# Performance work log

Hardware: AMD Instinct MI355X
Metric: run time of the kernel (lower is better)

Reference implementation:

```python
import jax, jax.numpy as jnp
import numpy as np

EMB = 1024
HID = 4 * EMB
HEADS = 16
HEAD_DIM = EMB // HEADS


def gelu_tanh(x):
    c = jnp.sqrt(jnp.asarray(2.0 / jnp.pi, x.dtype))
    return 0.5 * x * (1.0 + jnp.tanh(c * (x + 0.044715 * x ** 3)))


def layernorm(x, scale, shift, eps=1e-5):
    mean = jnp.mean(x, axis=-1, keepdims=True)
    var = jnp.var(x, axis=-1, keepdims=True)
    return scale * (x - mean) / jnp.sqrt(var + eps) + shift


def setup_inputs() -> dict:
    key = jax.random.key(0)
    ks = jax.random.split(key, 12)
    s = 0.02
    return {
        "x": jax.random.normal(ks[0], (2, 2048, EMB), jnp.float32),
        "Wq": jax.random.normal(ks[1], (EMB, EMB), jnp.float32) * s,
        "Wk": jax.random.normal(ks[2], (EMB, EMB), jnp.float32) * s,
        "Wv": jax.random.normal(ks[3], (EMB, EMB), jnp.float32) * s,
        "Wo": jax.random.normal(ks[4], (EMB, EMB), jnp.float32) * s,
        "bo": jnp.zeros((EMB,), jnp.float32),
        "W1": jax.random.normal(ks[5], (EMB, HID), jnp.float32) * s,
        "b1": jnp.zeros((HID,), jnp.float32),
        "W2": jax.random.normal(ks[6], (HID, EMB), jnp.float32) * s,
        "b2": jnp.zeros((EMB,), jnp.float32),
        "ln1_scale": jnp.ones((EMB,), jnp.float32),
        "ln1_shift": jnp.zeros((EMB,), jnp.float32),
        "ln2_scale": jnp.ones((EMB,), jnp.float32),
        "ln2_shift": jnp.zeros((EMB,), jnp.float32),
    }


def reference(x, Wq, Wk, Wv, Wo, bo, W1, b1, W2, b2,
              ln1_scale, ln1_shift, ln2_scale, ln2_shift):
    B, S, D = x.shape

    # pre-norm attention + residual
    h = layernorm(x, ln1_scale, ln1_shift)
    q = (h @ Wq).reshape(B, S, HEADS, HEAD_DIM).transpose(0, 2, 1, 3)  # bhsd
    k = (h @ Wk).reshape(B, S, HEADS, HEAD_DIM).transpose(0, 2, 1, 3)
    v = (h @ Wv).reshape(B, S, HEADS, HEAD_DIM).transpose(0, 2, 1, 3)

    scores = jnp.einsum("bhqd,bhkd->bhqk", q, k)
    causal = jnp.tril(jnp.ones((S, S), bool))
    scores = jnp.where(causal, scores, -jnp.inf)
    attn = jax.nn.softmax(scores / jnp.sqrt(jnp.asarray(HEAD_DIM, x.dtype)), axis=-1)
    ctx = jnp.einsum("bhqk,bhkd->bhqd", attn, v)
    ctx = ctx.transpose(0, 2, 1, 3).reshape(B, S, D)
    x = x + (ctx @ Wo + bo)

    # pre-norm FFN + residual
    h = layernorm(x, ln2_scale, ln2_shift)
    h = gelu_tanh(h @ W1 + b1) @ W2 + b2
    return x + h
```

## Files before the change

kernel.cpp:

```cpp
#include <hip/hip_runtime.h>
#include <hip/hip_bf16.h>
#include <stdint.h>

#define B_   2
#define S_   2048
#define D_   1024
#define H_   16
#define DH_  64
#define HID_ 4096
#define M_   4096

typedef __bf16 bf16x8 __attribute__((ext_vector_type(8)));
typedef float  f32x4  __attribute__((ext_vector_type(4)));
typedef float  f32x16 __attribute__((ext_vector_type(16)));
typedef uint32_t u32x4v __attribute__((ext_vector_type(4)));

typedef const uint32_t __attribute__((address_space(1))) u32g;
typedef uint32_t       __attribute__((address_space(3))) u32l;

#define SCL2K_ 0.18033688011112042f

__device__ __forceinline__ uint16_t f2bf(float f) {
  uint32_t u = __builtin_bit_cast(uint32_t, f);
  u += 0x7FFFu + ((u >> 16) & 1u);
  return (uint16_t)(u >> 16);
}

__device__ __forceinline__ float bf2f(uint16_t u) {
  return __builtin_bit_cast(float, (uint32_t)u << 16);
}

__device__ __forceinline__ void gload_lds16(const void* g, void* l) {
  __builtin_amdgcn_global_load_lds((u32g*)g, (u32l*)l, 16, 0, 0);
}

__device__ __forceinline__ const bf16x8* lds8p(const uint16_t* base, int row,
                                               int cole) {
  int byt = (cole * 2) ^ ((row & 7) << 4);
  return reinterpret_cast<const bf16x8*>(base + row * 64 + (byt >> 1));
}

__device__ __forceinline__ uint32_t cvtpk_bf16(float lo, float hi) {
  uint32_t d;
  asm("v_cvt_pk_bf16_f32 %0, %1, %2" : "=v"(d) : "v"(lo), "v"(hi));
  return d;
}
__device__ __forceinline__ void pl32swap(uint32_t& a, uint32_t& b) {
  asm volatile("v_permlane32_swap_b32 %0, %1" : "+v"(a), "+v"(b));
}

__global__ void wconv_t(const float* __restrict__ W, uint16_t* __restrict__ WT,
                        int K, int N) {
  __shared__ float tile[32][33];
  int n0 = blockIdx.x * 32, k0 = blockIdx.y * 32;
  int tx = threadIdx.x, ty = threadIdx.y;
#pragma unroll
  for (int i = 0; i < 4; ++i)
    tile[ty + i * 8][tx] = W[(size_t)(k0 + ty + i * 8) * N + n0 + tx];
  __syncthreads();
#pragma unroll
  for (int i = 0; i < 4; ++i)
    WT[(size_t)(n0 + ty + i * 8) * K + k0 + tx] = f2bf(tile[tx][ty + i * 8]);
}

__global__ __launch_bounds__(256) void ln_k(const float* __restrict__ x,
                                            const float* __restrict__ sc,
                                            const float* __restrict__ sh,
                                            uint16_t* __restrict__ out) {
  int row = blockIdx.x;
  int t = threadIdx.x;
  float4 v = reinterpret_cast<const float4*>(x + (size_t)row * D_)[t];
  float s = v.x + v.y + v.z + v.w;
  float ss = v.x * v.x + v.y * v.y + v.z * v.z + v.w * v.w;
#pragma unroll
  for (int off = 32; off >= 1; off >>= 1) {
    s += __shfl_xor(s, off);
    ss += __shfl_xor(ss, off);
  }
  __shared__ float red[8];
  int wid = t >> 6, lane = t & 63;
  if (lane == 0) { red[wid] = s; red[wid + 4] = ss; }
  __syncthreads();
  s = red[0] + red[1] + red[2] + red[3];
  ss = red[4] + red[5] + red[6] + red[7];
  float mean = s * (1.0f / D_);
  float var = ss * (1.0f / D_) - mean * mean;
  float rstd = rsqrtf(var + 1e-5f);
  float4 g = reinterpret_cast<const float4*>(sc)[t];
  float4 b = reinterpret_cast<const float4*>(sh)[t];
  ushort4 o;
  o.x = f2bf(g.x * (v.x - mean) * rstd + b.x);
  o.y = f2bf(g.y * (v.y - mean) * rstd + b.y);
  o.z = f2bf(g.z * (v.z - mean) * rstd + b.z);
  o.w = f2bf(g.w * (v.w - mean) * rstd + b.w);
  reinterpret_cast<ushort4*>(out + (size_t)row * D_)[t] = o;
}

__global__ __launch_bounds__(256) void reduce4_k(
    const uint16_t* __restrict__ P0, const uint16_t* __restrict__ P1,
    const uint16_t* __restrict__ P2, const uint16_t* __restrict__ P3,
    const float* __restrict__ resid, const float* __restrict__ bias,
    float* __restrict__ out) {
  int row = blockIdx.x, t = threadIdx.x;
  size_t base = (size_t)row * D_ + t * 4;
  float4 r = *reinterpret_cast<const float4*>(resid + base);
  float4 b = reinterpret_cast<const float4*>(bias)[t];
  ushort4 u0 = *reinterpret_cast<const ushort4*>(P0 + base);
  ushort4 u1 = *reinterpret_cast<const ushort4*>(P1 + base);
  ushort4 u2 = *reinterpret_cast<const ushort4*>(P2 + base);
  ushort4 u3 = *reinterpret_cast<const ushort4*>(P3 + base);
  float4 o;
  o.x = r.x + b.x + bf2f(u0.x) + bf2f(u1.x) + bf2f(u2.x) + bf2f(u3.x);
  o.y = r.y + b.y + bf2f(u0.y) + bf2f(u1.y) + bf2f(u2.y) + bf2f(u3.y);
  o.z = r.z + b.z + bf2f(u0.z) + bf2f(u1.z) + bf2f(u2.z) + bf2f(u3.z);
  o.w = r.w + b.w + bf2f(u0.w) + bf2f(u1.w) + bf2f(u2.w) + bf2f(u3.w);
  *reinterpret_cast<float4*>(out + base) = o;
}

__global__ void vtrans_k(const uint16_t* __restrict__ V, uint16_t* __restrict__ VT) {
  __shared__ uint16_t tile[32][33];
  int s0 = blockIdx.x * 32, d0 = blockIdx.y * 32, bh = blockIdx.z;
  int tx = threadIdx.x, ty = threadIdx.y;
  const uint16_t* vb = V + (size_t)bh * S_ * DH_;
  uint16_t* vtb = VT + (size_t)bh * DH_ * S_;
#pragma unroll
  for (int i = 0; i < 4; ++i)
    tile[ty + i * 8][tx] = vb[(size_t)(s0 + ty + i * 8) * DH_ + d0 + tx];
  __syncthreads();
#pragma unroll
  for (int i = 0; i < 4; ++i)
    vtb[(size_t)(d0 + ty + i * 8) * S_ + s0 + tx] = tile[tx][ty + i * 8];
}

template <int EPI>
__global__ __launch_bounds__(512, 2) void gemm8(
    const uint16_t* __restrict__ A, const uint16_t* __restrict__ BT,
    void* __restrict__ Cout, const float* __restrict__ bias,
    uint16_t* __restrict__ P0, uint16_t* __restrict__ P1,
    uint16_t* __restrict__ P2, uint16_t* __restrict__ P3,
    int M, int N, int K) {
  __shared__ uint16_t As[2][2][128 * 64];
  __shared__ uint16_t Bs[2][2][128 * 64];
  int t = threadIdx.x;
  int lane = t & 63, wid = t >> 6;
  int wm = wid >> 2, wn = wid & 3;
  int l15 = lane & 15, lk8 = (lane >> 4) * 8, lr4 = (lane >> 4) * 4;
  int gx = gridDim.x;
  int nwg = gx * gridDim.y;
  int bid = blockIdx.y * gx + blockIdx.x;
  int swz = (bid & 7) * (nwg >> 3) + (bid >> 3);
  int bx = swz % gx, by = swz / gx;
  int m0 = by * 256, n0 = bx * 256;
  int ksz = K / gridDim.z;
  int kbeg = blockIdx.z * ksz;
  int NT = ksz >> 6;

  int r0 = t >> 3, slot0 = t & 7;
  int scol = (slot0 ^ (r0 & 7)) * 8;

  auto STAGE_A = [&](int kt, int half, int buf) {
    const uint16_t* src =
        A + (size_t)(m0 + half * 128 + r0) * K + kbeg + kt * 64 + scol;
    uint16_t* dst = &As[buf][half][t * 8];
    gload_lds16(src, dst);
    gload_lds16(src + (size_t)64 * K, dst + 4096);
  };
  auto STAGE_B = [&](int kt, int half, int buf) {
    const uint16_t* src =
        BT + (size_t)(n0 + half * 128 + r0) * K + kbeg + kt * 64 + scol;
    uint16_t* dst = &Bs[buf][half][t * 8];
    gload_lds16(src, dst);
    gload_lds16(src + (size_t)64 * K, dst + 4096);
  };

  bf16x8 a[4][2], b[2][2];
  auto LDA = [&](int buf, int mh) {
#pragma unroll
    for (int j = 0; j < 4; ++j)
#pragma unroll
      for (int kk = 0; kk < 2; ++kk)
        a[j][kk] = *lds8p(As[buf][mh], wm * 64 + j * 16 + l15, kk * 32 + lk8);
  };
  auto LDB = [&](int buf, int nh) {
#pragma unroll
    for (int jj = 0; jj < 2; ++jj)
#pragma unroll
      for (int kk = 0; kk < 2; ++kk)
        b[jj][kk] = *lds8p(Bs[buf][nh], wn * 32 + jj * 16 + l15, kk * 32 + lk8);
  };

  f32x4 acc[8][4] = {};
  auto MM = [&](int mh, int nh) {
    __builtin_amdgcn_s_setprio(1);
#pragma unroll
    for (int kk = 0; kk < 2; ++kk)
#pragma unroll
      for (int j = 0; j < 4; ++j)
#pragma unroll
        for (int jj = 0; jj < 2; ++jj)
          acc[mh * 4 + j][nh * 2 + jj] = __builtin_amdgcn_mfma_f32_16x16x32_bf16(
              a[j][kk], b[jj][kk], acc[mh * 4 + j][nh * 2 + jj], 0, 0, 0);
    __builtin_amdgcn_s_setprio(0);
  };
  auto BAR = [&]() {
    __builtin_amdgcn_s_barrier();
    asm volatile("" ::: "memory");
  };
  auto LGKM0 = [&]() {
    asm volatile("s_waitcnt lgkmcnt(0)" ::: "memory");
    __builtin_amdgcn_sched_barrier(0);
  };

  STAGE_A(0, 0, 0);
  STAGE_B(0, 1, 0);
  STAGE_B(0, 0, 0);
  STAGE_A(0, 1, 0);
  STAGE_A(1, 0, 1);
  STAGE_B(1, 1, 1);
  asm volatile("s_waitcnt vmcnt(4)" ::: "memory");
  BAR();

  for (int T = 0; T < NT; ++T) {
    int cur = T & 1;
    LDA(cur, 0);
    LDB(cur, 0);
    if (T + 1 < NT) STAGE_B(T + 1, 0, cur ^ 1);
    BAR(); LGKM0();
    MM(0, 0);
    BAR();
    LDB(cur, 1);
    if (T + 1 < NT) STAGE_A(T + 1, 1, cur ^ 1);
    BAR(); LGKM0();
    MM(0, 1);
    BAR();
    LDA(cur, 1);
    if (T + 2 < NT) STAGE_A(T + 2, 0, cur);
    BAR(); LGKM0();
    MM(1, 1);
    BAR();
    LDB(cur, 0);
    if (T + 2 < NT) STAGE_B(T + 2, 1, cur);
    BAR(); LGKM0();
    MM(1, 0);
    if (T + 1 < NT) {
      if (T == NT - 2) {
        asm volatile("s_waitcnt vmcnt(0)" ::: "memory");
      } else {
        asm volatile("s_waitcnt vmcnt(4)" ::: "memory");
      }
    }
    BAR();
  }

  uint16_t* Pz = nullptr;
  if constexpr (EPI == 3) {
    int z = blockIdx.z;
    Pz = (z == 0) ? P0 : (z == 1) ? P1 : (z == 2) ? P2 : P3;
  }
#pragma unroll
  for (int mi = 0; mi < 8; ++mi) {
#pragma unroll
    for (int ni = 0; ni < 4; ++ni) {
#pragma unroll
      for (int rr = 0; rr < 4; ++rr) {
        int gm = m0 + (mi >> 2) * 128 + wm * 64 + (mi & 3) * 16 + lr4 + rr;
        int gn = n0 + (ni >> 1) * 128 + wn * 32 + (ni & 1) * 16 + l15;
        float v = acc[mi][ni][rr];
        if constexpr (EPI == 0) {
          int which = gn >> 10, nc = gn & 1023;
          int h = nc >> 6, dh = nc & 63;
          int bb = gm >> 11, s = gm & 2047;
          if (which == 1) v *= SCL2K_;
          ((uint16_t*)Cout)[((size_t)which * 32 + bb * 16 + h) * (S_ * 64) +
                            (size_t)s * 64 + dh] = f2bf(v);
        } else if constexpr (EPI == 2) {
          float u = v + bias[gn];
          float y = 0.7978845608028654f * (u + 0.044715f * u * u * u);
          float e = __expf(2.0f * y);
          float th = 1.0f - 2.0f / (e + 1.0f);
          ((uint16_t*)Cout)[(size_t)gm * N + gn] = f2bf(0.5f * u * (1.0f + th));
        } else {
          Pz[(size_t)gm * N + gn] = f2bf(v);
        }
      }
    }
  }
}

template <int EPI>
__global__ __launch_bounds__(256) void gemm_bt(
    const uint16_t* __restrict__ A, const uint16_t* __restrict__ BT,
    void* __restrict__ Cout, const float* __restrict__ bias,
    const float* __restrict__ resid, int M, int N, int K) {
  __shared__ uint16_t Asm_[128 * 64];
  __shared__ uint16_t Bsm_[128 * 64];
  int t = threadIdx.x;
  int lane = t & 63, wid = t >> 6;
  int wr = wid >> 1, wc = wid & 1;
  int nwg = gridDim.x * gridDim.y;
  int bid = blockIdx.y * gridDim.x + blockIdx.x;
  int swz = (bid & 7) * (nwg >> 3) + (bid >> 3);
  int bx = swz % gridDim.x, by = swz / gridDim.x;
  int m0 = by * 128, n0 = bx * 128;
  int l15 = lane & 15, lk8 = (lane >> 4) * 8;
  f32x4 acc[4][4] = {};

  auto STAGE = [&](int k0) {
#pragma unroll
    for (int it = 0; it < 4; ++it) {
      int idx = it * 256 + t;
      int r = idx >> 3, slot = idx & 7;
      int c = (slot ^ (r & 7)) * 8;
      gload_lds16(A + (size_t)(m0 + r) * K + k0 + c, &Asm_[idx * 8]);
      gload_lds16(BT + (size_t)(n0 + r) * K + k0 + c, &Bsm_[idx * 8]);
    }
  };

  int niter = K >> 6;
  for (int ki = 0; ki < niter; ++ki) {
    __syncthreads();
    STAGE(ki * 64);
    __syncthreads();
#pragma unroll
    for (int kk = 0; kk < 2; ++kk) {
      bf16x8 a[4], b[4];
#pragma unroll
      for (int mi = 0; mi < 4; ++mi)
        a[mi] = *lds8p(Asm_, wr * 64 + mi * 16 + l15, kk * 32 + lk8);
#pragma unroll
      for (int ni = 0; ni < 4; ++ni)
        b[ni] = *lds8p(Bsm_, wc * 64 + ni * 16 + l15, kk * 32 + lk8);
#pragma unroll
      for (int mi = 0; mi < 4; ++mi)
#pragma unroll
        for (int ni = 0; ni < 4; ++ni)
          acc[mi][ni] = __builtin_amdgcn_mfma_f32_16x16x32_bf16(
              a[mi], b[ni], acc[mi][ni], 0, 0, 0);
    }
  }
  int lr4 = (lane >> 4) * 4;
#pragma unroll
  for (int mi = 0; mi < 4; ++mi) {
#pragma unroll
    for (int ni = 0; ni < 4; ++ni) {
#pragma unroll
      for (int r = 0; r < 4; ++r) {
        int gm = m0 + wr * 64 + mi * 16 + lr4 + r;
        int gn = n0 + wc * 64 + ni * 16 + l15;
        float v = acc[mi][ni][r];
        if constexpr (EPI == 1) {
          ((float*)Cout)[(size_t)gm * N + gn] =
              resid[(size_t)gm * N + gn] + v + bias[gn];
        }
      }
    }
  }
}

__global__ __launch_bounds__(64) void attn32_k(const uint16_t* __restrict__ Q,
                                               const uint16_t* __restrict__ Kv,
                                               const uint16_t* __restrict__ VT,
                                               uint16_t* __restrict__ ctx) {
  __shared__ uint16_t Ksm[2][32 * 64];
  __shared__ uint16_t Vsm[2][32 * 64];
  __shared__ float invLDS[2][32];
  int bid = blockIdx.x;
  int wgrp = bid >> 3;
  int j = wgrp & 31;
  int bh = (bid & 7) + 8 * (wgrp >> 5);
  int lane = threadIdx.x;
  int l31 = lane & 31, lh = lane >> 5;
  int b_ = bh >> 4, h_ = bh & 15;

  auto STAGE = [&](int k0, int bufi) {
#pragma unroll
    for (int c = 0; c < 4; ++c) {
      int idx = c * 64 + lane;
      int r = idx >> 3, sl = idx & 7;
      int slp = sl ^ (r & 7);
      gload_lds16(Kv + ((size_t)bh * S_ + k0 + r) * 64 + slp * 8,
                  &Ksm[bufi][idx * 8]);
      int dh = 2 * r + (slp >> 2), ko = (slp & 3) * 8;
      gload_lds16(VT + ((size_t)bh * 64 + dh) * S_ + k0 + ko,
                  &Vsm[bufi][idx * 8]);
    }
  };

  int buf = 0;
  STAGE(0, 0);

  for (int half = 0; half < 2; ++half) {
    int qt = half ? (63 - j) : j;
    int nkt = qt + 1;
    int qbase = qt * 32;
    bf16x8 qf[4];
#pragma unroll
    for (int dk = 0; dk < 4; ++dk)
      qf[dk] = *reinterpret_cast<const bf16x8*>(
          Q + ((size_t)bh * S_ + qbase + l31) * 64 + dk * 16 + lh * 8);
    f32x16 o0 = {}, o1 = {};
    float mrow = -3.0e38f, lsum = 0.0f;

    for (int t = 0; t < nkt; ++t) {
      if (t + 1 < nkt) {
        STAGE((t + 1) * 32, buf ^ 1);
        asm volatile("s_waitcnt vmcnt(8)" ::: "memory");
      } else if (half == 0) {
        STAGE(0, buf ^ 1);
        asm volatile("s_waitcnt vmcnt(8)" ::: "memory");
      } else {
        asm volatile("s_waitcnt vmcnt(0)" ::: "memory");
      }
      __builtin_amdgcn_sched_barrier(0);
      f32x16 Sf = {};
#pragma unroll
      for (int dk = 0; dk < 4; ++dk) {
        bf16x8 kf = *lds8p(Ksm[buf], l31, dk * 16 + lh * 8);
        Sf = __builtin_amdgcn_mfma_f32_32x32x16_bf16(kf, qf[dk], Sf, 0, 0, 0);
      }
      float sv[16];
      if (t == nkt - 1) {
#pragma unroll
        for (int rr = 0; rr < 16; ++rr) {
          int koff = (rr & 3) + 8 * (rr >> 2) + 4 * lh;
          sv[rr] = (koff <= l31) ? Sf[rr] : -3.0e38f;
        }
      } else {
#pragma unroll
        for (int rr = 0; rr < 16; ++rr) sv[rr] = Sf[rr];
      }
      float mt = sv[0];
#pragma unroll
      for (int rr = 1; rr < 16; ++rr) mt = fmaxf(mt, sv[rr]);
#pragma unroll
      for (int off = 32; off >= 1; off >>= 1)
        mt = fmaxf(mt, __shfl_xor(mt, off));
      if (mt > mrow + 8.0f) {
        float fac = __builtin_amdgcn_exp2f(mrow - mt);
        mrow = mt;
        lsum *= fac;
#pragma unroll
        for (int rr = 0; rr < 16; ++rr) { o0[rr] *= fac; o1[rr] *= fac; }
      }
      float pv[16];
#pragma unroll
      for (int rr = 0; rr < 16; ++rr) {
        pv[rr] = __builtin_amdgcn_exp2f(sv[rr] - mrow);
        lsum += pv[rr];
      }
      uint32_t a0 = cvtpk_bf16(pv[0], pv[1]), b0 = cvtpk_bf16(pv[4], pv[5]);
      pl32swap(a0, b0);
      uint32_t a1 = cvtpk_bf16(pv[2], pv[3]), b1 = cvtpk_bf16(pv[6], pv[7]);
      pl32swap(a1, b1);
      u32x4v w0 = {a0, a1, b0, b1};
      bf16x8 pa0 = __builtin_bit_cast(bf16x8, w0);
      uint32_t a2 = cvtpk_bf16(pv[8], pv[9]), b2 = cvtpk_bf16(pv[12], pv[13]);
      pl32swap(a2, b2);
      uint32_t a3 = cvtpk_bf16(pv[10], pv[11]), b3 = cvtpk_bf16(pv[14], pv[15]);
      pl32swap(a3, b3);
      u32x4v w1 = {a2, a3, b2, b3};
      bf16x8 pa1 = __builtin_bit_cast(bf16x8, w1);
      int vrow = l31 >> 1, vcb = (l31 & 1) * 32 + lh * 8;
      bf16x8 v00 = *lds8p(Vsm[buf], vrow, vcb);
      o0 = __builtin_amdgcn_mfma_f32_32x32x16_bf16(pa0, v00, o0, 0, 0, 0);
      bf16x8 v01 = *lds8p(Vsm[buf], vrow, vcb + 16);
      o0 = __builtin_amdgcn_mfma_f32_32x32x16_bf16(pa1, v01, o0, 0, 0, 0);
      bf16x8 v10 = *lds8p(Vsm[buf], 16 + vrow, vcb);
      o1 = __builtin_amdgcn_mfma_f32_32x32x16_bf16(pa0, v10, o1, 0, 0, 0);
      bf16x8 v11 = *lds8p(Vsm[buf], 16 + vrow, vcb + 16);
      o1 = __builtin_amdgcn_mfma_f32_32x32x16_bf16(pa1, v11, o1, 0, 0, 0);
      buf ^= 1;
    }
    lsum += __shfl_xor(lsum, 32);
    if (lane < 32) invLDS[half][l31] = 1.0f / lsum;
    asm volatile("s_waitcnt lgkmcnt(0)" ::: "memory");
    __builtin_amdgcn_sched_barrier(0);
    float inv[16];
#pragma unroll
    for (int rr = 0; rr < 16; ++rr)
      inv[rr] = invLDS[half][(rr & 3) + 8 * (rr >> 2) + 4 * lh];
#pragma unroll
    for (int rr = 0; rr < 16; ++rr) {
      int s = qbase + (rr & 3) + 8 * (rr >> 2) + 4 * lh;
      size_t base = ((size_t)(b_ * S_ + s)) * D_ + h_ * 64;
      ctx[base + l31] = f2bf(o0[rr] * inv[rr]);
      ctx[base + 32 + l31] = f2bf(o1[rr] * inv[rr]);
    }
  }
}

extern "C" void kernel_launch(void* const* d_in, const int* in_sizes, int n_in,
                              void* d_out, int out_size, void* d_ws, size_t ws_size,
                              hipStream_t stream) {
  const float* x    = (const float*)d_in[0];
  const float* Wq   = (const float*)d_in[1];
  const float* Wk   = (const float*)d_in[2];
  const float* Wv   = (const float*)d_in[3];
  const float* Wo   = (const float*)d_in[4];
  const float* bo   = (const float*)d_in[5];
  const float* W1   = (const float*)d_in[6];
  const float* b1   = (const float*)d_in[7];
  const float* W2   = (const float*)d_in[8];
  const float* b2   = (const float*)d_in[9];
  const float* ln1s = (const float*)d_in[10];
  const float* ln1b = (const float*)d_in[11];
  const float* ln2s = (const float*)d_in[12];
  const float* ln2b = (const float*)d_in[13];
  float* out = (float*)d_out;
  char* ws = (char*)d_ws;

  const size_t MB = 1024 * 1024;
  uint16_t* WQKVT = (uint16_t*)(ws + 0);
  uint16_t* WOT   = (uint16_t*)(ws + 6 * MB);
  uint16_t* W1T   = (uint16_t*)(ws + 8 * MB);
  uint16_t* W2T   = (uint16_t*)(ws + 16 * MB);
  uint16_t* H1    = (uint16_t*)(ws + 24 * MB);
  float*    X1    = (float*)(ws + 32 * MB);
  uint16_t* QKV   = (uint16_t*)(ws + 48 * MB);
  uint16_t* VTb   = (uint16_t*)(ws + 72 * MB);
  uint16_t* CTX   = (uint16_t*)(ws + 80 * MB);
  uint16_t* FFH   = (uint16_t*)(ws + 48 * MB);
  uint16_t* SP0   = (uint16_t*)(ws + 0);
  uint16_t* SP1   = (uint16_t*)(ws + 8 * MB);
  uint16_t* SP2   = (uint16_t*)(ws + 24 * MB);
  uint16_t* SP3   = (uint16_t*)(ws + 80 * MB);

  dim3 b32x8(32, 8);
  wconv_t<<<dim3(32, 32), b32x8, 0, stream>>>(Wq, WQKVT, 1024, 1024);
  wconv_t<<<dim3(32, 32), b32x8, 0, stream>>>(Wk, WQKVT + 1024 * 1024, 1024, 1024);
  wconv_t<<<dim3(32, 32), b32x8, 0, stream>>>(Wv, WQKVT + 2 * 1024 * 1024, 1024, 1024);
  wconv_t<<<dim3(32, 32), b32x8, 0, stream>>>(Wo, WOT, 1024, 1024);
  wconv_t<<<dim3(128, 32), b32x8, 0, stream>>>(W1, W1T, 1024, 4096);
  wconv_t<<<dim3(32, 128), b32x8, 0, stream>>>(W2, W2T, 4096, 1024);

  ln_k<<<M_, 256, 0, stream>>>(x, ln1s, ln1b, H1);
  gemm8<0><<<dim3(12, 16), 512, 0, stream>>>(H1, WQKVT, QKV, nullptr,
                                             nullptr, nullptr, nullptr, nullptr,
                                             M_, 3072, 1024);
  const uint16_t* Qp = QKV;
  const uint16_t* Kp = QKV + (size_t)32 * S_ * 64;
  const uint16_t* Vp = QKV + (size_t)64 * S_ * 64;
  vtrans_k<<<dim3(64, 2, 32), b32x8, 0, stream>>>(Vp, VTb);
  attn32_k<<<dim3(1024), 64, 0, stream>>>(Qp, Kp, VTb, CTX);
  gemm_bt<1><<<dim3(8, 32), 256, 0, stream>>>(CTX, WOT, X1, bo, x, M_, 1024, 1024);
  ln_k<<<M_, 256, 0, stream>>>(X1, ln2s, ln2b, H1);
  gemm8<2><<<dim3(16, 16), 512, 0, stream>>>(H1, W1T, FFH, b1,
                                             nullptr, nullptr, nullptr, nullptr,
                                             M_, 4096, 1024);
  gemm8<3><<<dim3(4, 16, 4), 512, 0, stream>>>(FFH, W2T, nullptr, nullptr,
                                               SP0, SP1, SP2, SP3,
                                               M_, 1024, 4096);
  reduce4_k<<<M_, 256, 0, stream>>>(SP0, SP1, SP2, SP3, X1, b2, out);
}
```

Measured before the change: 269.7 us.

## Split paired causal attention blocks into one q-tile per block, tweak swizzle and rescale

The attention kernel stops giving each block two complementary query tiles (j and 63-j) for load balance. It now launches one block per query tile, doubling the grid to 2048 single-wave blocks, with heavy tiles scheduled last by block index. The LDS swizzle gains an extra XOR bit on row bit 3 to cut bank conflicts, and the online-softmax rescale check now uses a wave-wide __any before the cross-lane max reduction. This trades the explicit pairing for more parallelism and leaves it to the hardware scheduler to balance the uneven causal work.

New measurement: 256.5 us. 4.9% less time.

```diff
diff --git a/kernel.cpp b/kernel.cpp
--- a/kernel.cpp
+++ b/kernel.cpp
@@ -37,6 +37,12 @@
 __device__ __forceinline__ const bf16x8* lds8p(const uint16_t* base, int row,
                                                int cole) {
   int byt = (cole * 2) ^ ((row & 7) << 4);
+  return reinterpret_cast<const bf16x8*>(base + row * 64 + (byt >> 1));
+}
+
+__device__ __forceinline__ const bf16x8* lds8p32(const uint16_t* base, int row,
+                                                 int cole) {
+  int byt = (cole * 2) ^ ((row & 7) << 4) ^ ((row & 8) << 2);
   return reinterpret_cast<const bf16x8*>(base + row * 64 + (byt >> 1));
 }
 
@@ -363,11 +369,10 @@
                                                uint16_t* __restrict__ ctx) {
   __shared__ uint16_t Ksm[2][32 * 64];
   __shared__ uint16_t Vsm[2][32 * 64];
-  __shared__ float invLDS[2][32];
+  __shared__ float invLDS[32];
   int bid = blockIdx.x;
-  int wgrp = bid >> 3;
-  int j = wgrp & 31;
-  int bh = (bid & 7) + 8 * (wgrp >> 5);
+  int qt = bid >> 5;
+  int bh = bid & 31;
   int lane = threadIdx.x;
   int l31 = lane & 31, lh = lane >> 5;
   int b_ = bh >> 4, h_ = bh & 15;
@@ -377,7 +382,7 @@
     for (int c = 0; c < 4; ++c) {
       int idx = c * 64 + lane;
       int r = idx >> 3, sl = idx & 7;
-      int slp = sl ^ (r & 7);
+      int slp = sl ^ (r & 7) ^ ((r & 8) >> 2);
       gload_lds16(Kv + ((size_t)bh * S_ + k0 + r) * 64 + slp * 8,
                   &Ksm[bufi][idx * 8]);
       int dh = 2 * r + (slp >> 2), ko = (slp & 3) * 8;
@@ -386,106 +391,101 @@
     }
   };
 
+  int nkt = qt + 1;
+  int qbase = qt * 32;
+  bf16x8 qf[4];
+#pragma unroll
+  for (int dk = 0; dk < 4; ++dk)
+    qf[dk] = *reinterpret_cast<const bf16x8*>(
+        Q + ((size_t)bh * S_ + qbase + l31) * 64 + dk * 16 + lh * 8);
+  f32x16 o0 = {}, o1 = {};
+  float mrow = -3.0e38f, lsum = 0.0f;
   int buf = 0;
   STAGE(0, 0);
 
-  for (int half = 0; half < 2; ++half) {
-    int qt = half ? (63 - j) : j;
-    int nkt = qt + 1;
-    int qbase = qt * 32;
-    bf16x8 qf[4];
-#pragma unroll
-    for (int dk = 0; dk < 4; ++dk)
-      qf[dk] = *reinterpret_cast<const bf16x8*>(
-          Q + ((size_t)bh * S_ + qbase + l31) * 64 + dk * 16 + lh * 8);
-    f32x16 o0 = {}, o1 = {};
-    float mrow = -3.0e38f, lsum = 0.0f;
-
-    for (int t = 0; t < nkt; ++t) {
-      if (t + 1 < nkt) {
-        STAGE((t + 1) * 32, buf ^ 1);
-        asm volatile("s_waitcnt vmcnt(8)" ::: "memory");
-      } else if (half == 0) {
-        STAGE(0, buf ^ 1);
-        asm volatile("s_waitcnt vmcnt(8)" ::: "memory");
-      } else {
-        asm volatile("s_waitcnt vmcnt(0)" ::: "memory");
+  for (int t = 0; t < nkt; ++t) {
+    if (t + 1 < nkt) {
+      STAGE((t + 1) * 32, buf ^ 1);
+      asm volatile("s_waitcnt vmcnt(8)" ::: "memory");
+    } else {
+      asm volatile("s_waitcnt vmcnt(0)" ::: "memory");
+    }
+    __builtin_amdgcn_sched_barrier(0);
+    f32x16 Sf = {};
+#pragma unroll
+    for (int dk = 0; dk < 4; ++dk) {
+      bf16x8 kf = *lds8p32(Ksm[buf], l31, dk * 16 + lh * 8);
+      Sf = __builtin_amdgcn_mfma_f32_32x32x16_bf16(kf, qf[dk], Sf, 0, 0, 0);
+    }
+    float sv[16];
+    if (t == nkt - 1) {
+#pragma unroll
+      for (int rr = 0; rr < 16; ++rr) {
+        int koff = (rr & 3) + 8 * (rr >> 2) + 4 * lh;
+        sv[rr] = (koff <= l31) ? Sf[rr] : -3.0e38f;
       }
-      __builtin_amdgcn_sched_barrier(0);
-      f32x16 Sf = {};
-#pragma unroll
-      for (int dk = 0; dk < 4; ++dk) {
-        bf16x8 kf = *lds8p(Ksm[buf], l31, dk * 16 + lh * 8);
-        Sf = __builtin_amdgcn_mfma_f32_32x32x16_bf16(kf, qf[dk], Sf, 0, 0, 0);
-      }
-      float sv[16];
-      if (t == nkt - 1) {
-#pragma unroll
-        for (int rr = 0; rr < 16; ++rr) {
-          int koff = (rr & 3) + 8 * (rr >> 2) + 4 * lh;
-          sv[rr] = (koff <= l31) ? Sf[rr] : -3.0e38f;
-        }
-      } else {
-#pragma unroll
-        for (int rr = 0; rr < 16; ++rr) sv[rr] = Sf[rr];
-      }
-      float mt = sv[0];
-#pragma unroll
-      for (int rr = 1; rr < 16; ++rr) mt = fmaxf(mt, sv[rr]);
+    } else {
+#pragma unroll
+      for (int rr = 0; rr < 16; ++rr) sv[rr] = Sf[rr];
+    }
+    float mt16 = sv[0];
+#pragma unroll
+    for (int rr = 1; rr < 16; ++rr) mt16 = fmaxf(mt16, sv[rr]);
+    if (__any(mt16 > mrow + 8.0f)) {
+      float mt = mt16;
 #pragma unroll
       for (int off = 32; off >= 1; off >>= 1)
         mt = fmaxf(mt, __shfl_xor(mt, off));
-      if (mt > mrow + 8.0f) {
-        float fac = __builtin_amdgcn_exp2f(mrow - mt);
-        mrow = mt;
-        lsum *= fac;
-#pragma unroll
-        for (int rr = 0; rr < 16; ++rr) { o0[rr] *= fac; o1[rr] *= fac; }
-      }
-      float pv[16];
-#pragma unroll
-      for (int rr = 0; rr < 16; ++rr) {
-        pv[rr] = __builtin_amdgcn_exp2f(sv[rr] - mrow);
-        lsum += pv[rr];
-      }
-      uint32_t a0 = cvtpk_bf16(pv[0], pv[1]), b0 = cvtpk_bf16(pv[4], pv[5]);
-      pl32swap(a0, b0);
-      uint32_t a1 = cvtpk_bf16(pv[2], pv[3]), b1 = cvtpk_bf16(pv[6], pv[7]);
-      pl32swap(a1, b1);
-      u32x4v w0 = {a0, a1, b0, b1};
-      bf16x8 pa0 = __builtin_bit_cast(bf16x8, w0);
-      uint32_t a2 = cvtpk_bf16(pv[8], pv[9]), b2 = cvtpk_bf16(pv[12], pv[13]);
-      pl32swap(a2, b2);
-      uint32_t a3 = cvtpk_bf16(pv[10], pv[11]), b3 = cvtpk_bf16(pv[14], pv[15]);
-      pl32swap(a3, b3);
-      u32x4v w1 = {a2, a3, b2, b3};
-      bf16x8 pa1 = __builtin_bit_cast(bf16x8, w1);
-      int vrow = l31 >> 1, vcb = (l31 & 1) * 32 + lh * 8;
-      bf16x8 v00 = *lds8p(Vsm[buf], vrow, vcb);
-      o0 = __builtin_amdgcn_mfma_f32_32x32x16_bf16(pa0, v00, o0, 0, 0, 0);
-      bf16x8 v01 = *lds8p(Vsm[buf], vrow, vcb + 16);
-      o0 = __builtin_amdgcn_mfma_f32_32x32x16_bf16(pa1, v01, o0, 0, 0, 0);
-      bf16x8 v10 = *lds8p(Vsm[buf], 16 + vrow, vcb);
-      o1 = __builtin_amdgcn_mfma_f32_32x32x16_bf16(pa0, v10, o1, 0, 0, 0);
-      bf16x8 v11 = *lds8p(Vsm[buf], 16 + vrow, vcb + 16);
-      o1 = __builtin_amdgcn_mfma_f32_32x32x16_bf16(pa1, v11, o1, 0, 0, 0);
-      buf ^= 1;
-    }
-    lsum += __shfl_xor(lsum, 32);
-    if (lane < 32) invLDS[half][l31] = 1.0f / lsum;
-    asm volatile("s_waitcnt lgkmcnt(0)" ::: "memory");
-    __builtin_amdgcn_sched_barrier(0);
-    float inv[16];
-#pragma unroll
-    for (int rr = 0; rr < 16; ++rr)
-      inv[rr] = invLDS[half][(rr & 3) + 8 * (rr >> 2) + 4 * lh];
+      mt = fmaxf(mt, mrow);
+      float fac = __builtin_amdgcn_exp2f(mrow - mt);
+      mrow = mt;
+      lsum *= fac;
+#pragma unroll
+      for (int rr = 0; rr < 16; ++rr) { o0[rr] *= fac; o1[rr] *= fac; }
+    }
+    float pv[16];
 #pragma unroll
     for (int rr = 0; rr < 16; ++rr) {
-      int s = qbase + (rr & 3) + 8 * (rr >> 2) + 4 * lh;
-      size_t base = ((size_t)(b_ * S_ + s)) * D_ + h_ * 64;
-      ctx[base + l31] = f2bf(o0[rr] * inv[rr]);
-      ctx[base + 32 + l31] = f2bf(o1[rr] * inv[rr]);
-    }
+      pv[rr] = __builtin_amdgcn_exp2f(sv[rr] - mrow);
+      lsum += pv[rr];
+    }
+    uint32_t a0 = cvtpk_bf16(pv[0], pv[1]), b0 = cvtpk_bf16(pv[4], pv[5]);
+    pl32swap(a0, b0);
+    uint32_t a1 = cvtpk_bf16(pv[2], pv[3]), b1 = cvtpk_bf16(pv[6], pv[7]);
+    pl32swap(a1, b1);
+    u32x4v w0 = {a0, a1, b0, b1};
+    bf16x8 pa0 = __builtin_bit_cast(bf16x8, w0);
+    uint32_t a2 = cvtpk_bf16(pv[8], pv[9]), b2 = cvtpk_bf16(pv[12], pv[13]);
+    pl32swap(a2, b2);
+    uint32_t a3 = cvtpk_bf16(pv[10], pv[11]), b3 = cvtpk_bf16(pv[14], pv[15]);
+    pl32swap(a3, b3);
+    u32x4v w1 = {a2, a3, b2, b3};
+    bf16x8 pa1 = __builtin_bit_cast(bf16x8, w1);
+    int vrow = l31 >> 1, vcb = (l31 & 1) * 32 + lh * 8;
+    bf16x8 v00 = *lds8p32(Vsm[buf], vrow, vcb);
+    o0 = __builtin_amdgcn_mfma_f32_32x32x16_bf16(pa0, v00, o0, 0, 0, 0);
+    bf16x8 v01 = *lds8p32(Vsm[buf], vrow, vcb + 16);
+    o0 = __builtin_amdgcn_mfma_f32_32x32x16_bf16(pa1, v01, o0, 0, 0, 0);
+    bf16x8 v10 = *lds8p32(Vsm[buf], 16 + vrow, vcb);
+    o1 = __builtin_amdgcn_mfma_f32_32x32x16_bf16(pa0, v10, o1, 0, 0, 0);
+    bf16x8 v11 = *lds8p32(Vsm[buf], 16 + vrow, vcb + 16);
+    o1 = __builtin_amdgcn_mfma_f32_32x32x16_bf16(pa1, v11, o1, 0, 0, 0);
+    buf ^= 1;
+  }
+  lsum += __shfl_xor(lsum, 32);
+  if (lane < 32) invLDS[l31] = 1.0f / lsum;
+  asm volatile("s_waitcnt lgkmcnt(0)" ::: "memory");
+  __builtin_amdgcn_sched_barrier(0);
+  float inv[16];
+#pragma unroll
+  for (int rr = 0; rr < 16; ++rr)
+    inv[rr] = invLDS[(rr & 3) + 8 * (rr >> 2) + 4 * lh];
+#pragma unroll
+  for (int rr = 0; rr < 16; ++rr) {
+    int s = qbase + (rr & 3) + 8 * (rr >> 2) + 4 * lh;
+    size_t base = ((size_t)(b_ * S_ + s)) * D_ + h_ * 64;
+    ctx[base + l31] = f2bf(o0[rr] * inv[rr]);
+    ctx[base + 32 + l31] = f2bf(o1[rr] * inv[rr]);
   }
 }
 
@@ -541,7 +541,7 @@
   const uint16_t* Kp = QKV + (size_t)32 * S_ * 64;
   const uint16_t* Vp = QKV + (size_t)64 * S_ * 64;
   vtrans_k<<<dim3(64, 2, 32), b32x8, 0, stream>>>(Vp, VTb);
-  attn32_k<<<dim3(1024), 64, 0, stream>>>(Qp, Kp, VTb, CTX);
+  attn32_k<<<dim3(2048), 64, 0, stream>>>(Qp, Kp, VTb, CTX);
   gemm_bt<1><<<dim3(8, 32), 256, 0, stream>>>(CTX, WOT, X1, bo, x, M_, 1024, 1024);
   ln_k<<<M_, 256, 0, stream>>>(X1, ln2s, ln2b, H1);
   gemm8<2><<<dim3(16, 16), 512, 0, stream>>>(H1, W1T, FFH, b1,
```
